# Kernel optimization log

Measured on AMD Instinct MI355X. Metric: run time of the kernel, lower is better.

The kernel has to match this reference:

```python
import jax, jax.numpy as jnp
import numpy as np

B, C, H, W_ = 64, 512, 32, 32


def setup_inputs() -> dict:
    key = jax.random.key(0)
    k0, k1, k2, k3 = jax.random.split(key, 4)
    x = jax.random.normal(k0, (B, C, H, W_), dtype=jnp.float32)
    # conv1x1 weight [3c, c] (kernel dims of size 1 squeezed)
    W = jax.random.normal(k1, (3 * C, C), dtype=jnp.float32) * 0.02
    rel_h = jax.random.normal(k2, (1, C, H, 1), dtype=jnp.float32)
    rel_w = jax.random.normal(k3, (1, C, 1, W_), dtype=jnp.float32)
    return {"x": x, "W": W, "rel_h": rel_h, "rel_w": rel_w}


def reference(x, W, rel_h, rel_w):
    b, c, h, w = x.shape
    n = h * w
    xf = x.reshape(b, c, n)
    # 1x1 conv == channel matmul: [b, 3c, n]
    qkv = jnp.einsum('oc,bcn->bon', W, xf)
    q, k, v = jnp.split(qkv, 3, axis=1)  # each [b, c, n]
    # content-content: q^T k -> [b, n, n]
    content_content = jnp.einsum('bcn,bcm->bnm', q, k)
    # relative position bias: pos [c, n]; pos^T @ q -> [b, n, n]
    pos = (rel_h + rel_w).reshape(c, n)
    content_position = jnp.einsum('cn,bcm->bnm', pos, q)
    attention = jax.nn.softmax(content_content + content_position, axis=-1)
    # out = bmm(v, attention^T) -> [b, c, n]
    out = jnp.einsum('bcm,bnm->bcn', v, attention)
    return out.reshape(b, c, h, w)
```

## Files before the change

kernel.cpp:

```cpp
#include <hip/hip_runtime.h>

#define B_    64
#define C_    512
#define H_    32
#define WDIM  32
#define N_    1024
#define M3C   1536

typedef unsigned short ushort_t;
typedef __attribute__((ext_vector_type(8))) short bf16x8;
typedef __attribute__((ext_vector_type(4))) float f32x4;

__device__ __forceinline__ ushort_t f2bf(float x) {
    unsigned u = __float_as_uint(x);
    unsigned r = (u + 0x7FFFu + ((u >> 16) & 1u)) >> 16;
    return (ushort_t)r;
}
__device__ __forceinline__ float bf2f(ushort_t b) {
    return __uint_as_float(((unsigned)b) << 16);
}
__device__ __forceinline__ void split_write(float v, ushort_t* __restrict__ ph,
                                            ushort_t* __restrict__ pl, size_t idx) {
    ushort_t hb = f2bf(v);
    ph[idx] = hb;
    pl[idx] = f2bf(v - bf2f(hb));
}

__device__ __forceinline__ void gld16(const void* g, void* l) {
    __builtin_amdgcn_global_load_lds((const __attribute__((address_space(1))) unsigned int*)g,
                                     (__attribute__((address_space(3))) unsigned int*)l,
                                     16, 0, 0);
}

__global__ __launch_bounds__(256) void pos_kernel(const float* __restrict__ rel_h,
                                                  const float* __restrict__ rel_w,
                                                  float* __restrict__ pos) {
    int idx = blockIdx.x * 256 + threadIdx.x;
    if (idx >= C_ * N_) return;
    int c = idx >> 10;
    int n = idx & (N_ - 1);
    int h = n >> 5;
    int w = n & (WDIM - 1);
    pos[idx] = rel_h[c * H_ + h] + rel_w[c * WDIM + w];
}

__global__ __launch_bounds__(256) void mmT_f32(const float* __restrict__ A, int lda,
                                               const float* __restrict__ B, int ldb,
                                               float* __restrict__ D, int ldd, int K) {
    __shared__ float As[16][64];
    __shared__ float Bs[16][64];
    const int m0 = blockIdx.y * 64;
    const int n0 = blockIdx.x * 64;
    const int tx = threadIdx.x, ty = threadIdx.y;
    const int tid = ty * 16 + tx;
    float acc[4][4] = {};
    for (int k0 = 0; k0 < K; k0 += 16) {
        #pragma unroll
        for (int t = 0; t < 4; ++t) {
            int e = tid + t * 256;
            int j = e >> 6, i = e & 63;
            As[j][i] = A[(size_t)(k0 + j) * lda + m0 + i];
            Bs[j][i] = B[(size_t)(k0 + j) * ldb + n0 + i];
        }
        __syncthreads();
        #pragma unroll
        for (int kk = 0; kk < 16; ++kk) {
            float a[4], bb[4];
            #pragma unroll
            for (int i = 0; i < 4; ++i) a[i]  = As[kk][ty * 4 + i];
            #pragma unroll
            for (int j = 0; j < 4; ++j) bb[j] = Bs[kk][tx * 4 + j];
            #pragma unroll
            for (int i = 0; i < 4; ++i)
                #pragma unroll
                for (int j = 0; j < 4; ++j)
                    acc[i][j] += a[i] * bb[j];
        }
        __syncthreads();
    }
    #pragma unroll
    for (int i = 0; i < 4; ++i)
        #pragma unroll
        for (int j = 0; j < 4; ++j)
            D[(size_t)(m0 + ty * 4 + i) * ldd + n0 + tx * 4 + j] = acc[i][j];
}

__global__ __launch_bounds__(256) void f_split(const float* __restrict__ Mtmp,
                                               const float* __restrict__ Wm,
                                               ushort_t* __restrict__ Fh,
                                               ushort_t* __restrict__ Fl) {
    int idx = blockIdx.x * 256 + threadIdx.x;
    if (idx >= 1024 * C_) return;
    int o = idx >> 9;
    int c = idx & (C_ - 1);
    float v = (o < 512) ? Mtmp[idx] : Wm[(size_t)(512 + o) * C_ + c];
    split_write(v, Fh, Fl, idx);
}

__global__ __launch_bounds__(256) void xT_split(const float* __restrict__ x,
                                                ushort_t* __restrict__ xh,
                                                ushort_t* __restrict__ xl) {
    __shared__ float t[32][33];
    const int bl = blockIdx.z;
    const int c0 = blockIdx.y * 32;
    const int n0 = blockIdx.x * 32;
    const float* xb = x + (size_t)bl * C_ * N_;
    ushort_t* xhb = xh + (size_t)bl * N_ * C_;
    ushort_t* xlb = xl + (size_t)bl * N_ * C_;
    const int tx = threadIdx.x & 31, ty = threadIdx.x >> 5;
    #pragma unroll
    for (int r = 0; r < 4; ++r)
        t[ty + r * 8][tx] = xb[(size_t)(c0 + ty + r * 8) * N_ + n0 + tx];
    __syncthreads();
    #pragma unroll
    for (int r = 0; r < 4; ++r) {
        float v = t[tx][ty + r * 8];
        size_t o = (size_t)(n0 + ty + r * 8) * C_ + c0 + tx;
        split_write(v, xhb, xlb, o);
    }
}


__global__ __launch_bounds__(512, 2) void g1_mfma(const ushort_t* __restrict__ Fh_,
                                                  const ushort_t* __restrict__ Fl_,
                                                  const ushort_t* __restrict__ xTh_,
                                                  const ushort_t* __restrict__ xTl_,
                                                  ushort_t* __restrict__ tTh_,
                                                  ushort_t* __restrict__ tTl_,
                                                  ushort_t* __restrict__ vh_,
                                                  ushort_t* __restrict__ vl_) {
    __shared__ ushort_t lds[2][4][2][4096];
    const int bl = blockIdx.z;
    const int n0 = blockIdx.x * 256;
    const int m0 = blockIdx.y * 256;
    const char* Ah = (const char*)Fh_;
    const char* Al = (const char*)Fl_;
    const char* Bh = (const char*)(xTh_ + (size_t)bl * N_ * C_);
    const char* Bl = (const char*)(xTl_ + (size_t)bl * N_ * C_);

    const int tid = threadIdx.x;
    const int lane = tid & 63, wid = tid >> 6;
    const int wr = wid >> 2, wc = wid & 3;
    const int lr = lane & 15, g = lane >> 4;
    const int cswz = g ^ ((lr >> 1) & 3);
    const int offA = lr * 32 + cswz * 8;
    const int offB = ((wc & 1) * 64 + lr) * 32 + cswz * 8;
    const int srow = tid >> 2;
    const int toff = srow * 1024 + (((tid & 3) ^ ((srow >> 1) & 3)) << 4);
    const int ldst = wid * 512;

    f32x4 acc[8][4] = {};

#define G1_ISSUE_A(buf, kb) \
    gld16(Ah + (size_t)(m0)       * 1024 + (kb) + toff, &lds[buf][0][0][ldst]); \
    gld16(Ah + (size_t)(m0 + 128) * 1024 + (kb) + toff, &lds[buf][0][1][ldst]); \
    gld16(Al + (size_t)(m0)       * 1024 + (kb) + toff, &lds[buf][1][0][ldst]); \
    gld16(Al + (size_t)(m0 + 128) * 1024 + (kb) + toff, &lds[buf][1][1][ldst]);
#define G1_ISSUE_B(buf, kb) \
    gld16(Bh + (size_t)(n0)       * 1024 + (kb) + toff, &lds[buf][2][0][ldst]); \
    gld16(Bh + (size_t)(n0 + 128) * 1024 + (kb) + toff, &lds[buf][2][1][ldst]); \
    gld16(Bl + (size_t)(n0)       * 1024 + (kb) + toff, &lds[buf][3][0][ldst]); \
    gld16(Bl + (size_t)(n0 + 128) * 1024 + (kb) + toff, &lds[buf][3][1][ldst]);

    G1_ISSUE_A(0, 0);
    G1_ISSUE_B(0, 0);
    asm volatile("s_waitcnt vmcnt(0)" ::: "memory");
    __builtin_amdgcn_s_barrier();

    bf16x8 bfh[4], bfl[4];
    for (int t = 0; t < 16; ++t) {
        const int cur = t & 1, nxt = cur ^ 1;
        const bool pf = (t < 15);
        const int nk = (t + 1) * 64;
        #pragma unroll
        for (int p = 0; p < 4; ++p) {
            if (p == 0) {
                #pragma unroll
                for (int j = 0; j < 4; ++j) {
                    bfh[j] = *(const bf16x8*)&lds[cur][2][wc >> 1][j * 512 + offB];
                    bfl[j] = *(const bf16x8*)&lds[cur][3][wc >> 1][j * 512 + offB];
                }
            }
            bf16x8 ah0 = *(const bf16x8*)&lds[cur][0][wr][(p * 2 + 0) * 512 + offA];
            bf16x8 al0 = *(const bf16x8*)&lds[cur][1][wr][(p * 2 + 0) * 512 + offA];
            bf16x8 ah1 = *(const bf16x8*)&lds[cur][0][wr][(p * 2 + 1) * 512 + offA];
            bf16x8 al1 = *(const bf16x8*)&lds[cur][1][wr][(p * 2 + 1) * 512 + offA];
            if (pf && p == 0) { G1_ISSUE_A(nxt, nk); }
            if (pf && p == 1) { G1_ISSUE_B(nxt, nk); }
            __builtin_amdgcn_s_barrier();
            asm volatile("s_waitcnt lgkmcnt(0)" ::: "memory");
            __builtin_amdgcn_s_setprio(1);
            #pragma unroll
            for (int j = 0; j < 4; ++j) {
                acc[p*2+0][j] = __builtin_amdgcn_mfma_f32_16x16x32_bf16(ah0, bfh[j], acc[p*2+0][j], 0,0,0);
                acc[p*2+0][j] = __builtin_amdgcn_mfma_f32_16x16x32_bf16(ah0, bfl[j], acc[p*2+0][j], 0,0,0);
                acc[p*2+0][j] = __builtin_amdgcn_mfma_f32_16x16x32_bf16(al0, bfh[j], acc[p*2+0][j], 0,0,0);
                acc[p*2+1][j] = __builtin_amdgcn_mfma_f32_16x16x32_bf16(ah1, bfh[j], acc[p*2+1][j], 0,0,0);
                acc[p*2+1][j] = __builtin_amdgcn_mfma_f32_16x16x32_bf16(ah1, bfl[j], acc[p*2+1][j], 0,0,0);
                acc[p*2+1][j] = __builtin_amdgcn_mfma_f32_16x16x32_bf16(al1, bfh[j], acc[p*2+1][j], 0,0,0);
            }
            __builtin_amdgcn_s_setprio(0);
            if (p == 3) asm volatile("s_waitcnt vmcnt(0)" ::: "memory");
            __builtin_amdgcn_s_barrier();
        }
    }
#undef G1_ISSUE_A
#undef G1_ISSUE_B

    if (m0 < 512) {
        ushort_t* th = tTh_ + (size_t)bl * N_ * C_;
        ushort_t* tl = tTl_ + (size_t)bl * N_ * C_;
        #pragma unroll
        for (int i = 0; i < 8; ++i) {
            int ob = m0 + wr * 128 + i * 16 + g * 4;
            #pragma unroll
            for (int j = 0; j < 4; ++j) {
                int n = n0 + wc * 64 + j * 16 + lr;
                ushort4 h4, l4;
                ushort_t hb;
                float v0 = acc[i][j][0], v1 = acc[i][j][1], v2 = acc[i][j][2], v3 = acc[i][j][3];
                hb = f2bf(v0); h4.x = hb; l4.x = f2bf(v0 - bf2f(hb));
                hb = f2bf(v1); h4.y = hb; l4.y = f2bf(v1 - bf2f(hb));
                hb = f2bf(v2); h4.z = hb; l4.z = f2bf(v2 - bf2f(hb));
                hb = f2bf(v3); h4.w = hb; l4.w = f2bf(v3 - bf2f(hb));
                *reinterpret_cast<ushort4*>(&th[(size_t)n * C_ + ob]) = h4;
                *reinterpret_cast<ushort4*>(&tl[(size_t)n * C_ + ob]) = l4;
            }
        }
    } else {
        ushort_t* vh = vh_ + (size_t)bl * C_ * N_;
        ushort_t* vl = vl_ + (size_t)bl * C_ * N_;
        #pragma unroll
        for (int i = 0; i < 8; ++i) {
            int cb = m0 - 512 + wr * 128 + i * 16 + g * 4;
            #pragma unroll
            for (int j = 0; j < 4; ++j) {
                int m = n0 + wc * 64 + j * 16 + lr;
                #pragma unroll
                for (int r = 0; r < 4; ++r) {
                    float v = acc[i][j][r];
                    ushort_t hb = f2bf(v);
                    vh[(size_t)(cb + r) * N_ + m] = hb;
                    vl[(size_t)(cb + r) * N_ + m] = f2bf(v - bf2f(hb));
                }
            }
        }
    }
}

__global__ __launch_bounds__(512, 2) void g2_mfma(const ushort_t* __restrict__ xTh_,
                                                  const ushort_t* __restrict__ xTl_,
                                                  const ushort_t* __restrict__ rTh_,
                                                  const ushort_t* __restrict__ rTl_,
                                                  const ushort_t* __restrict__ tTh_,
                                                  const ushort_t* __restrict__ tTl_,
                                                  float* __restrict__ S) {
    __shared__ ushort_t lds[2][4][2][4096];
    const int bl = blockIdx.z;
    const int m0 = blockIdx.x * 256;
    const int n0 = blockIdx.y * 256;
    const char* xh = (const char*)(xTh_ + (size_t)bl * N_ * C_);
    const char* xl = (const char*)(xTl_ + (size_t)bl * N_ * C_);
    const char* th = (const char*)(tTh_ + (size_t)bl * N_ * C_);
    const char* tl = (const char*)(tTl_ + (size_t)bl * N_ * C_);
    const char* rh = (const char*)rTh_;
    const char* rl = (const char*)rTl_;

    const int tid = threadIdx.x;
    const int lane = tid & 63, wid = tid >> 6;
    const int wr = wid >> 2, wc = wid & 3;
    const int lr = lane & 15, g = lane >> 4;
    const int cswz = g ^ ((lr >> 1) & 3);
    const int offA = lr * 32 + cswz * 8;
    const int offB = ((wc & 1) * 64 + lr) * 32 + cswz * 8;
    const int srow = tid >> 2;
    const int toff = srow * 1024 + (((tid & 3) ^ ((srow >> 1) & 3)) << 4);
    const int ldst = wid * 512;

    f32x4 acc[8][4] = {};

#define G2_SRC(s, vAh, vAl, vBh, vBl, vk) \
    const char *vAh, *vAl, *vBh, *vBl; int vk; \
    if ((s) < 16) { vAh = xh; vAl = xl; vBh = th; vBl = tl; vk = (s) * 64; } \
    else          { vAh = rh; vAl = rl; vBh = xh; vBl = xl; vk = ((s) - 16) * 64; }
#define G2_ISSUE_A(buf, vAh, vAl, vk) \
    gld16(vAh + (size_t)(n0)       * 1024 + (vk) + toff, &lds[buf][0][0][ldst]); \
    gld16(vAh + (size_t)(n0 + 128) * 1024 + (vk) + toff, &lds[buf][0][1][ldst]); \
    gld16(vAl + (size_t)(n0)       * 1024 + (vk) + toff, &lds[buf][1][0][ldst]); \
    gld16(vAl + (size_t)(n0 + 128) * 1024 + (vk) + toff, &lds[buf][1][1][ldst]);
#define G2_ISSUE_B(buf, vBh, vBl, vk) \
    gld16(vBh + (size_t)(m0)       * 1024 + (vk) + toff, &lds[buf][2][0][ldst]); \
    gld16(vBh + (size_t)(m0 + 128) * 1024 + (vk) + toff, &lds[buf][2][1][ldst]); \
    gld16(vBl + (size_t)(m0)       * 1024 + (vk) + toff, &lds[buf][3][0][ldst]); \
    gld16(vBl + (size_t)(m0 + 128) * 1024 + (vk) + toff, &lds[buf][3][1][ldst]);

    {
        G2_SRC(0, pAh, pAl, pBh, pBl, pk);
        G2_ISSUE_A(0, pAh, pAl, pk);
        G2_ISSUE_B(0, pBh, pBl, pk);
        asm volatile("s_waitcnt vmcnt(0)" ::: "memory");
        __builtin_amdgcn_s_barrier();
    }

    bf16x8 bfh[4], bfl[4];
    for (int t = 0; t < 32; ++t) {
        const int cur = t & 1, nxt = cur ^ 1;
        const bool pf = (t < 31);
        G2_SRC(t + 1, nAh, nAl, nBh, nBl, nk);
        #pragma unroll
        for (int p = 0; p < 4; ++p) {
            if (p == 0) {
                #pragma unroll
                for (int j = 0; j < 4; ++j) {
                    bfh[j] = *(const bf16x8*)&lds[cur][2][wc >> 1][j * 512 + offB];
                    bfl[j] = *(const bf16x8*)&lds[cur][3][wc >> 1][j * 512 + offB];
                }
            }
            bf16x8 ah0 = *(const bf16x8*)&lds[cur][0][wr][(p * 2 + 0) * 512 + offA];
            bf16x8 al0 = *(const bf16x8*)&lds[cur][1][wr][(p * 2 + 0) * 512 + offA];
            bf16x8 ah1 = *(const bf16x8*)&lds[cur][0][wr][(p * 2 + 1) * 512 + offA];
            bf16x8 al1 = *(const bf16x8*)&lds[cur][1][wr][(p * 2 + 1) * 512 + offA];
            if (pf && p == 0) { G2_ISSUE_A(nxt, nAh, nAl, nk); }
            if (pf && p == 1) { G2_ISSUE_B(nxt, nBh, nBl, nk); }
            __builtin_amdgcn_s_barrier();
            asm volatile("s_waitcnt lgkmcnt(0)" ::: "memory");
            __builtin_amdgcn_s_setprio(1);
            #pragma unroll
            for (int j = 0; j < 4; ++j) {
                acc[p*2+0][j] = __builtin_amdgcn_mfma_f32_16x16x32_bf16(ah0, bfh[j], acc[p*2+0][j], 0,0,0);
                acc[p*2+0][j] = __builtin_amdgcn_mfma_f32_16x16x32_bf16(ah0, bfl[j], acc[p*2+0][j], 0,0,0);
                acc[p*2+0][j] = __builtin_amdgcn_mfma_f32_16x16x32_bf16(al0, bfh[j], acc[p*2+0][j], 0,0,0);
                acc[p*2+1][j] = __builtin_amdgcn_mfma_f32_16x16x32_bf16(ah1, bfh[j], acc[p*2+1][j], 0,0,0);
                acc[p*2+1][j] = __builtin_amdgcn_mfma_f32_16x16x32_bf16(ah1, bfl[j], acc[p*2+1][j], 0,0,0);
                acc[p*2+1][j] = __builtin_amdgcn_mfma_f32_16x16x32_bf16(al1, bfh[j], acc[p*2+1][j], 0,0,0);
            }
            __builtin_amdgcn_s_setprio(0);
            if (p == 3) asm volatile("s_waitcnt vmcnt(0)" ::: "memory");
            __builtin_amdgcn_s_barrier();
        }
    }
#undef G2_SRC
#undef G2_ISSUE_A
#undef G2_ISSUE_B

    float* Sb = S + (size_t)bl * N_ * N_;
    #pragma unroll
    for (int i = 0; i < 8; ++i) {
        int n = n0 + wr * 128 + i * 16 + g * 4;
        #pragma unroll
        for (int j = 0; j < 4; ++j) {
            int m = m0 + wc * 64 + j * 16 + lr;
            #pragma unroll
            for (int r = 0; r < 4; ++r)
                Sb[(size_t)(n + r) * N_ + m] = acc[i][j][r];
        }
    }
}

__device__ __forceinline__ float waveMax(float v) {
    #pragma unroll
    for (int o = 32; o > 0; o >>= 1) v = fmaxf(v, __shfl_down(v, o));
    return v;
}
__device__ __forceinline__ float waveSum(float v) {
    #pragma unroll
    for (int o = 32; o > 0; o >>= 1) v += __shfl_down(v, o);
    return v;
}

__global__ __launch_bounds__(256) void softmax_bf16(const float* __restrict__ S,
                                                    ushort_t* __restrict__ P) {
    const float* Sr = S + (size_t)blockIdx.x * N_;
    ushort_t* Pr = P + (size_t)blockIdx.x * N_;
    const int tid = threadIdx.x;
    float4 v = reinterpret_cast<const float4*>(Sr)[tid];
    __shared__ float redm[4];
    __shared__ float reds[4];
    const int wave = tid >> 6, lane = tid & 63;

    float m = fmaxf(fmaxf(v.x, v.y), fmaxf(v.z, v.w));
    m = waveMax(m);
    if (lane == 0) redm[wave] = m;
    __syncthreads();
    m = fmaxf(fmaxf(redm[0], redm[1]), fmaxf(redm[2], redm[3]));

    v.x = __expf(v.x - m); v.y = __expf(v.y - m);
    v.z = __expf(v.z - m); v.w = __expf(v.w - m);
    float s = v.x + v.y + v.z + v.w;
    s = waveSum(s);
    if (lane == 0) reds[wave] = s;
    __syncthreads();
    s = reds[0] + reds[1] + reds[2] + reds[3];
    const float inv = 1.0f / s;
    ushort4 p;
    p.x = f2bf(v.x * inv); p.y = f2bf(v.y * inv);
    p.z = f2bf(v.z * inv); p.w = f2bf(v.w * inv);
    reinterpret_cast<ushort4*>(Pr)[tid] = p;
}

__global__ __launch_bounds__(512, 2) void g4_mfma(const ushort_t* __restrict__ vh_,
                                                  const ushort_t* __restrict__ vl_,
                                                  const ushort_t* __restrict__ P_,
                                                  float* __restrict__ out) {
    __shared__ ushort_t lds[2][3][2][4096];
    const int bl = blockIdx.z;
    const int n0 = blockIdx.x * 256;
    const int c0 = blockIdx.y * 256;
    const char* Ah = (const char*)(vh_ + (size_t)bl * C_ * N_);
    const char* Al = (const char*)(vl_ + (size_t)bl * C_ * N_);
    const char* Bp = (const char*)(P_ + (size_t)bl * N_ * N_);

    const int tid = threadIdx.x;
    const int lane = tid & 63, wid = tid >> 6;
    const int wr = wid >> 2, wc = wid & 3;
    const int lr = lane & 15, g = lane >> 4;
    const int cswz = g ^ ((lr >> 1) & 3);
    const int offA = lr * 32 + cswz * 8;
    const int offB = ((wc & 1) * 64 + lr) * 32 + cswz * 8;
    const int srow = tid >> 2;
    const int toff = srow * 2048 + (((tid & 3) ^ ((srow >> 1) & 3)) << 4);
    const int ldst = wid * 512;

    f32x4 acc[8][4] = {};

#define G4_ISSUE_A(buf, kb) \
    gld16(Ah + (size_t)(c0)       * 2048 + (kb) + toff, &lds[buf][0][0][ldst]); \
    gld16(Ah + (size_t)(c0 + 128) * 2048 + (kb) + toff, &lds[buf][0][1][ldst]); \
    gld16(Al + (size_t)(c0)       * 2048 + (kb) + toff, &lds[buf][1][0][ldst]); \
    gld16(Al + (size_t)(c0 + 128) * 2048 + (kb) + toff, &lds[buf][1][1][ldst]);
#define G4_ISSUE_B(buf, kb) \
    gld16(Bp + (size_t)(n0)       * 2048 + (kb) + toff, &lds[buf][2][0][ldst]); \
    gld16(Bp + (size_t)(n0 + 128) * 2048 + (kb) + toff, &lds[buf][2][1][ldst]);

    G4_ISSUE_A(0, 0);
    G4_ISSUE_B(0, 0);
    asm volatile("s_waitcnt vmcnt(0)" ::: "memory");
    __builtin_amdgcn_s_barrier();

    bf16x8 bf[4];
    for (int t = 0; t < 32; ++t) {
        const int cur = t & 1, nxt = cur ^ 1;
        const bool pf = (t < 31);
        const int nk = (t + 1) * 64;
        #pragma unroll
        for (int p = 0; p < 4; ++p) {
            if (p == 0) {
                #pragma unroll
                for (int j = 0; j < 4; ++j)
                    bf[j] = *(const bf16x8*)&lds[cur][2][wc >> 1][j * 512 + offB];
            }
            bf16x8 ah0 = *(const bf16x8*)&lds[cur][0][wr][(p * 2 + 0) * 512 + offA];
            bf16x8 al0 = *(const bf16x8*)&lds[cur][1][wr][(p * 2 + 0) * 512 + offA];
            bf16x8 ah1 = *(const bf16x8*)&lds[cur][0][wr][(p * 2 + 1) * 512 + offA];
            bf16x8 al1 = *(const bf16x8*)&lds[cur][1][wr][(p * 2 + 1) * 512 + offA];
            if (pf && p == 0) { G4_ISSUE_A(nxt, nk); }
            if (pf && p == 1) { G4_ISSUE_B(nxt, nk); }
            __builtin_amdgcn_s_barrier();
            asm volatile("s_waitcnt lgkmcnt(0)" ::: "memory");
            __builtin_amdgcn_s_setprio(1);
            #pragma unroll
            for (int j = 0; j < 4; ++j) {
                acc[p*2+0][j] = __builtin_amdgcn_mfma_f32_16x16x32_bf16(ah0, bf[j], acc[p*2+0][j], 0,0,0);
                acc[p*2+0][j] = __builtin_amdgcn_mfma_f32_16x16x32_bf16(al0, bf[j], acc[p*2+0][j], 0,0,0);
                acc[p*2+1][j] = __builtin_amdgcn_mfma_f32_16x16x32_bf16(ah1, bf[j], acc[p*2+1][j], 0,0,0);
                acc[p*2+1][j] = __builtin_amdgcn_mfma_f32_16x16x32_bf16(al1, bf[j], acc[p*2+1][j], 0,0,0);
            }
            __builtin_amdgcn_s_setprio(0);
            if (p == 3) asm volatile("s_waitcnt vmcnt(0)" ::: "memory");
            __builtin_amdgcn_s_barrier();
        }
    }
#undef G4_ISSUE_A
#undef G4_ISSUE_B

    float* ob = out + (size_t)bl * C_ * N_;
    #pragma unroll
    for (int i = 0; i < 8; ++i) {
        int c = c0 + wr * 128 + i * 16 + g * 4;
        #pragma unroll
        for (int j = 0; j < 4; ++j) {
            int n = n0 + wc * 64 + j * 16 + lr;
            #pragma unroll
            for (int r = 0; r < 4; ++r)
                ob[(size_t)(c + r) * N_ + n] = acc[i][j][r];
        }
    }
}

extern "C" void kernel_launch(void* const* d_in, const int* in_sizes, int n_in,
                              void* d_out, int out_size, void* d_ws, size_t ws_size,
                              hipStream_t stream) {
    const float* x     = (const float*)d_in[0];
    const float* Wm    = (const float*)d_in[1];
    const float* rel_h = (const float*)d_in[2];
    const float* rel_w = (const float*)d_in[3];
    float* out = (float*)d_out;

    const size_t posB  = (size_t)C_ * N_ * 4;
    const size_t MtB   = (size_t)C_ * C_ * 4;
    const size_t rtB   = (size_t)C_ * N_ * 4;
    const size_t fplB  = (size_t)1024 * C_ * 2;
    const size_t rtplB = (size_t)N_ * C_ * 2;
    const size_t xtB   = (size_t)N_ * C_ * 2;
    const size_t ttB   = (size_t)N_ * C_ * 2;
    const size_t vplB  = (size_t)C_ * N_ * 2;
    const size_t sB    = (size_t)N_ * N_ * 4;
    const size_t pB    = (size_t)N_ * N_ * 2;
    const size_t per_batch = 2 * xtB + 2 * ttB + 2 * vplB + sB + pB;
    const size_t persist   = posB + MtB + rtB + 2 * fplB + 2 * rtplB;

    size_t rem = (ws_size > persist) ? (ws_size - persist) : 0;
    int chunkB = (int)(rem / per_batch);
    if (chunkB < 1)  chunkB = 1;
    if (chunkB > B_) chunkB = B_;

    char* p = (char*)d_ws;
    float*    pos  = (float*)p;    p += posB;
    float*    Mtmp = (float*)p;    p += MtB;
    float*    rtmp = (float*)p;    p += rtB;
    ushort_t* Fh   = (ushort_t*)p; p += fplB;
    ushort_t* Fl   = (ushort_t*)p; p += fplB;
    ushort_t* rTh  = (ushort_t*)p; p += rtplB;
    ushort_t* rTl  = (ushort_t*)p; p += rtplB;
    ushort_t* xTh  = (ushort_t*)p; p += (size_t)chunkB * xtB;
    ushort_t* xTl  = (ushort_t*)p; p += (size_t)chunkB * xtB;
    ushort_t* tTh  = (ushort_t*)p; p += (size_t)chunkB * ttB;
    ushort_t* tTl  = (ushort_t*)p; p += (size_t)chunkB * ttB;
    ushort_t* vh   = (ushort_t*)p; p += (size_t)chunkB * vplB;
    ushort_t* vl   = (ushort_t*)p; p += (size_t)chunkB * vplB;
    float*    S    = (float*)p;    p += (size_t)chunkB * sB;
    ushort_t* P    = (ushort_t*)p; p += (size_t)chunkB * pB;

    dim3 blk16(16, 16);
    pos_kernel<<<(C_ * N_ + 255) / 256, 256, 0, stream>>>(rel_h, rel_w, pos);
    mmT_f32<<<dim3(C_ / 64, C_ / 64), blk16, 0, stream>>>(Wm, C_, Wm + (size_t)C_ * C_, C_,
                                                          Mtmp, C_, C_);
    mmT_f32<<<dim3(N_ / 64, C_ / 64), blk16, 0, stream>>>(Wm, C_, pos, N_, rtmp, N_, C_);
    f_split<<<(1024 * C_ + 255) / 256, 256, 0, stream>>>(Mtmp, Wm, Fh, Fl);
    xT_split<<<dim3(N_ / 32, C_ / 32, 1), 256, 0, stream>>>(rtmp, rTh, rTl);

    for (int b0 = 0; b0 < B_; b0 += chunkB) {
        int nb = (b0 + chunkB <= B_) ? chunkB : (B_ - b0);
        const float* x_b   = x   + (size_t)b0 * C_ * N_;
        float*       out_b = out + (size_t)b0 * C_ * N_;
        xT_split<<<dim3(N_ / 32, C_ / 32, nb), 256, 0, stream>>>(x_b, xTh, xTl);
        g1_mfma<<<dim3(4, 4, nb), 512, 0, stream>>>(Fh, Fl, xTh, xTl, tTh, tTl, vh, vl);
        g2_mfma<<<dim3(4, 4, nb), 512, 0, stream>>>(xTh, xTl, rTh, rTl, tTh, tTl, S);
        softmax_bf16<<<nb * N_, 256, 0, stream>>>(S, P);
        g4_mfma<<<dim3(4, 2, nb), 512, 0, stream>>>(vh, vl, P, out_b);
    }
}
```

Baseline: 1.261 ms.

## Switch GEMM kernels to 32x32x16 MFMA with two-stage-ahead prefetch pipeline

```diff
diff --git a/kernel.cpp b/kernel.cpp
--- a/kernel.cpp
+++ b/kernel.cpp
@@ -10,6 +10,9 @@
 typedef unsigned short ushort_t;
 typedef __attribute__((ext_vector_type(8))) short bf16x8;
 typedef __attribute__((ext_vector_type(4))) float f32x4;
+typedef __attribute__((ext_vector_type(16))) float f32x16;
+
+#define MEMFENCE asm volatile("" ::: "memory")
 
 __device__ __forceinline__ ushort_t f2bf(float x) {
     unsigned u = __float_as_uint(x);
@@ -141,110 +144,114 @@
     const int tid = threadIdx.x;
     const int lane = tid & 63, wid = tid >> 6;
     const int wr = wid >> 2, wc = wid & 3;
-    const int lr = lane & 15, g = lane >> 4;
-    const int cswz = g ^ ((lr >> 1) & 3);
-    const int offA = lr * 32 + cswz * 8;
-    const int offB = ((wc & 1) * 64 + lr) * 32 + cswz * 8;
+    const int l31 = lane & 31, l5 = lane >> 5;
+    const int swz4 = (l31 >> 1) & 3;
+    const int chk0 = ((l5)     ^ swz4) << 3;
+    const int chk1 = ((2 | l5) ^ swz4) << 3;
     const int srow = tid >> 2;
     const int toff = srow * 1024 + (((tid & 3) ^ ((srow >> 1) & 3)) << 4);
     const int ldst = wid * 512;
 
-    f32x4 acc[8][4] = {};
-
-#define G1_ISSUE_A(buf, kb) \
+    f32x16 acc[4][2] = {};
+
+#define G1_ISSUE(buf, kb) \
     gld16(Ah + (size_t)(m0)       * 1024 + (kb) + toff, &lds[buf][0][0][ldst]); \
     gld16(Ah + (size_t)(m0 + 128) * 1024 + (kb) + toff, &lds[buf][0][1][ldst]); \
     gld16(Al + (size_t)(m0)       * 1024 + (kb) + toff, &lds[buf][1][0][ldst]); \
-    gld16(Al + (size_t)(m0 + 128) * 1024 + (kb) + toff, &lds[buf][1][1][ldst]);
-#define G1_ISSUE_B(buf, kb) \
+    gld16(Al + (size_t)(m0 + 128) * 1024 + (kb) + toff, &lds[buf][1][1][ldst]); \
     gld16(Bh + (size_t)(n0)       * 1024 + (kb) + toff, &lds[buf][2][0][ldst]); \
     gld16(Bh + (size_t)(n0 + 128) * 1024 + (kb) + toff, &lds[buf][2][1][ldst]); \
     gld16(Bl + (size_t)(n0)       * 1024 + (kb) + toff, &lds[buf][3][0][ldst]); \
     gld16(Bl + (size_t)(n0 + 128) * 1024 + (kb) + toff, &lds[buf][3][1][ldst]);
 
-    G1_ISSUE_A(0, 0);
-    G1_ISSUE_B(0, 0);
-    asm volatile("s_waitcnt vmcnt(0)" ::: "memory");
-    __builtin_amdgcn_s_barrier();
-
-    bf16x8 bfh[4], bfl[4];
+    G1_ISSUE(0, 0);
+    G1_ISSUE(1, 64);
+    int cur = 0;
     for (int t = 0; t < 16; ++t) {
-        const int cur = t & 1, nxt = cur ^ 1;
-        const bool pf = (t < 15);
-        const int nk = (t + 1) * 64;
-        #pragma unroll
-        for (int p = 0; p < 4; ++p) {
-            if (p == 0) {
-                #pragma unroll
-                for (int j = 0; j < 4; ++j) {
-                    bfh[j] = *(const bf16x8*)&lds[cur][2][wc >> 1][j * 512 + offB];
-                    bfl[j] = *(const bf16x8*)&lds[cur][3][wc >> 1][j * 512 + offB];
-                }
-            }
-            bf16x8 ah0 = *(const bf16x8*)&lds[cur][0][wr][(p * 2 + 0) * 512 + offA];
-            bf16x8 al0 = *(const bf16x8*)&lds[cur][1][wr][(p * 2 + 0) * 512 + offA];
-            bf16x8 ah1 = *(const bf16x8*)&lds[cur][0][wr][(p * 2 + 1) * 512 + offA];
-            bf16x8 al1 = *(const bf16x8*)&lds[cur][1][wr][(p * 2 + 1) * 512 + offA];
-            if (pf && p == 0) { G1_ISSUE_A(nxt, nk); }
-            if (pf && p == 1) { G1_ISSUE_B(nxt, nk); }
-            __builtin_amdgcn_s_barrier();
-            asm volatile("s_waitcnt lgkmcnt(0)" ::: "memory");
+        if (t + 1 < 16) asm volatile("s_waitcnt vmcnt(8)" ::: "memory");
+        else            asm volatile("s_waitcnt vmcnt(0)" ::: "memory");
+        __builtin_amdgcn_s_barrier();
+        MEMFENCE;
+        bf16x8 bh[2][2], bo[2][2];
+        #pragma unroll
+        for (int j = 0; j < 2; ++j) {
+            int br = ((wc & 1) * 64 + j * 32 + l31) * 32;
+            bh[j][0] = *(const bf16x8*)&lds[cur][2][wc >> 1][br + chk0];
+            bh[j][1] = *(const bf16x8*)&lds[cur][2][wc >> 1][br + chk1];
+            bo[j][0] = *(const bf16x8*)&lds[cur][3][wc >> 1][br + chk0];
+            bo[j][1] = *(const bf16x8*)&lds[cur][3][wc >> 1][br + chk1];
+        }
+        #pragma unroll
+        for (int i = 0; i < 4; ++i) {
+            int ar = (i * 32 + l31) * 32;
+            bf16x8 ah0 = *(const bf16x8*)&lds[cur][0][wr][ar + chk0];
+            bf16x8 ah1 = *(const bf16x8*)&lds[cur][0][wr][ar + chk1];
+            bf16x8 al0 = *(const bf16x8*)&lds[cur][1][wr][ar + chk0];
+            bf16x8 al1 = *(const bf16x8*)&lds[cur][1][wr][ar + chk1];
             __builtin_amdgcn_s_setprio(1);
             #pragma unroll
-            for (int j = 0; j < 4; ++j) {
-                acc[p*2+0][j] = __builtin_amdgcn_mfma_f32_16x16x32_bf16(ah0, bfh[j], acc[p*2+0][j], 0,0,0);
-                acc[p*2+0][j] = __builtin_amdgcn_mfma_f32_16x16x32_bf16(ah0, bfl[j], acc[p*2+0][j], 0,0,0);
-                acc[p*2+0][j] = __builtin_amdgcn_mfma_f32_16x16x32_bf16(al0, bfh[j], acc[p*2+0][j], 0,0,0);
-                acc[p*2+1][j] = __builtin_amdgcn_mfma_f32_16x16x32_bf16(ah1, bfh[j], acc[p*2+1][j], 0,0,0);
-                acc[p*2+1][j] = __builtin_amdgcn_mfma_f32_16x16x32_bf16(ah1, bfl[j], acc[p*2+1][j], 0,0,0);
-                acc[p*2+1][j] = __builtin_amdgcn_mfma_f32_16x16x32_bf16(al1, bfh[j], acc[p*2+1][j], 0,0,0);
+            for (int j = 0; j < 2; ++j) {
+                acc[i][j] = __builtin_amdgcn_mfma_f32_32x32x16_bf16(ah0, bh[j][0], acc[i][j], 0,0,0);
+                acc[i][j] = __builtin_amdgcn_mfma_f32_32x32x16_bf16(ah0, bo[j][0], acc[i][j], 0,0,0);
+                acc[i][j] = __builtin_amdgcn_mfma_f32_32x32x16_bf16(al0, bh[j][0], acc[i][j], 0,0,0);
+                acc[i][j] = __builtin_amdgcn_mfma_f32_32x32x16_bf16(ah1, bh[j][1], acc[i][j], 0,0,0);
+                acc[i][j] = __builtin_amdgcn_mfma_f32_32x32x16_bf16(ah1, bo[j][1], acc[i][j], 0,0,0);
+                acc[i][j] = __builtin_amdgcn_mfma_f32_32x32x16_bf16(al1, bh[j][1], acc[i][j], 0,0,0);
             }
             __builtin_amdgcn_s_setprio(0);
-            if (p == 3) asm volatile("s_waitcnt vmcnt(0)" ::: "memory");
-            __builtin_amdgcn_s_barrier();
-        }
-    }
-#undef G1_ISSUE_A
-#undef G1_ISSUE_B
+        }
+        asm volatile("s_waitcnt lgkmcnt(0)" ::: "memory");
+        __builtin_amdgcn_sched_barrier(0);
+        __builtin_amdgcn_s_barrier();
+        MEMFENCE;
+        if (t + 2 < 16) { G1_ISSUE(cur, (t + 2) * 64); }
+        cur ^= 1;
+    }
+#undef G1_ISSUE
 
     if (m0 < 512) {
         ushort_t* th = tTh_ + (size_t)bl * N_ * C_;
         ushort_t* tl = tTl_ + (size_t)bl * N_ * C_;
         #pragma unroll
-        for (int i = 0; i < 8; ++i) {
-            int ob = m0 + wr * 128 + i * 16 + g * 4;
-            #pragma unroll
-            for (int j = 0; j < 4; ++j) {
-                int n = n0 + wc * 64 + j * 16 + lr;
-                ushort4 h4, l4;
-                ushort_t hb;
-                float v0 = acc[i][j][0], v1 = acc[i][j][1], v2 = acc[i][j][2], v3 = acc[i][j][3];
-                hb = f2bf(v0); h4.x = hb; l4.x = f2bf(v0 - bf2f(hb));
-                hb = f2bf(v1); h4.y = hb; l4.y = f2bf(v1 - bf2f(hb));
-                hb = f2bf(v2); h4.z = hb; l4.z = f2bf(v2 - bf2f(hb));
-                hb = f2bf(v3); h4.w = hb; l4.w = f2bf(v3 - bf2f(hb));
-                *reinterpret_cast<ushort4*>(&th[(size_t)n * C_ + ob]) = h4;
-                *reinterpret_cast<ushort4*>(&tl[(size_t)n * C_ + ob]) = l4;
-            }
-        }
+        for (int i = 0; i < 4; ++i)
+            #pragma unroll
+            for (int j = 0; j < 2; ++j) {
+                int n = n0 + wc * 64 + j * 32 + l31;
+                #pragma unroll
+                for (int q = 0; q < 4; ++q) {
+                    int o = m0 + wr * 128 + i * 32 + q * 8 + l5 * 4;
+                    ushort4 h4, l4;
+                    ushort_t hb;
+                    float v0 = acc[i][j][q*4+0], v1 = acc[i][j][q*4+1];
+                    float v2 = acc[i][j][q*4+2], v3 = acc[i][j][q*4+3];
+                    hb = f2bf(v0); h4.x = hb; l4.x = f2bf(v0 - bf2f(hb));
+                    hb = f2bf(v1); h4.y = hb; l4.y = f2bf(v1 - bf2f(hb));
+                    hb = f2bf(v2); h4.z = hb; l4.z = f2bf(v2 - bf2f(hb));
+                    hb = f2bf(v3); h4.w = hb; l4.w = f2bf(v3 - bf2f(hb));
+                    *reinterpret_cast<ushort4*>(&th[(size_t)n * C_ + o]) = h4;
+                    *reinterpret_cast<ushort4*>(&tl[(size_t)n * C_ + o]) = l4;
+                }
+            }
     } else {
         ushort_t* vh = vh_ + (size_t)bl * C_ * N_;
         ushort_t* vl = vl_ + (size_t)bl * C_ * N_;
         #pragma unroll
-        for (int i = 0; i < 8; ++i) {
-            int cb = m0 - 512 + wr * 128 + i * 16 + g * 4;
-            #pragma unroll
-            for (int j = 0; j < 4; ++j) {
-                int m = n0 + wc * 64 + j * 16 + lr;
+        for (int i = 0; i < 4; ++i)
+            #pragma unroll
+            for (int j = 0; j < 2; ++j) {
+                int m = n0 + wc * 64 + j * 32 + l31;
                 #pragma unroll
-                for (int r = 0; r < 4; ++r) {
-                    float v = acc[i][j][r];
-                    ushort_t hb = f2bf(v);
-                    vh[(size_t)(cb + r) * N_ + m] = hb;
-                    vl[(size_t)(cb + r) * N_ + m] = f2bf(v - bf2f(hb));
+                for (int q = 0; q < 4; ++q) {
+                    int cb = m0 - 512 + wr * 128 + i * 32 + q * 8 + l5 * 4;
+                    #pragma unroll
+                    for (int rr = 0; rr < 4; ++rr) {
+                        float v = acc[i][j][q*4+rr];
+                        ushort_t hb = f2bf(v);
+                        vh[(size_t)(cb + rr) * N_ + m] = hb;
+                        vl[(size_t)(cb + rr) * N_ + m] = f2bf(v - bf2f(hb));
+                    }
                 }
             }
-        }
     }
 }
 
@@ -269,92 +276,93 @@
     const int tid = threadIdx.x;
     const int lane = tid & 63, wid = tid >> 6;
     const int wr = wid >> 2, wc = wid & 3;
-    const int lr = lane & 15, g = lane >> 4;
-    const int cswz = g ^ ((lr >> 1) & 3);
-    const int offA = lr * 32 + cswz * 8;
-    const int offB = ((wc & 1) * 64 + lr) * 32 + cswz * 8;
+    const int l31 = lane & 31, l5 = lane >> 5;
+    const int swz4 = (l31 >> 1) & 3;
+    const int chk0 = ((l5)     ^ swz4) << 3;
+    const int chk1 = ((2 | l5) ^ swz4) << 3;
     const int srow = tid >> 2;
     const int toff = srow * 1024 + (((tid & 3) ^ ((srow >> 1) & 3)) << 4);
     const int ldst = wid * 512;
 
-    f32x4 acc[8][4] = {};
-
-#define G2_SRC(s, vAh, vAl, vBh, vBl, vk) \
-    const char *vAh, *vAl, *vBh, *vBl; int vk; \
-    if ((s) < 16) { vAh = xh; vAl = xl; vBh = th; vBl = tl; vk = (s) * 64; } \
-    else          { vAh = rh; vAl = rl; vBh = xh; vBl = xl; vk = ((s) - 16) * 64; }
-#define G2_ISSUE_A(buf, vAh, vAl, vk) \
-    gld16(vAh + (size_t)(n0)       * 1024 + (vk) + toff, &lds[buf][0][0][ldst]); \
-    gld16(vAh + (size_t)(n0 + 128) * 1024 + (vk) + toff, &lds[buf][0][1][ldst]); \
-    gld16(vAl + (size_t)(n0)       * 1024 + (vk) + toff, &lds[buf][1][0][ldst]); \
-    gld16(vAl + (size_t)(n0 + 128) * 1024 + (vk) + toff, &lds[buf][1][1][ldst]);
-#define G2_ISSUE_B(buf, vBh, vBl, vk) \
-    gld16(vBh + (size_t)(m0)       * 1024 + (vk) + toff, &lds[buf][2][0][ldst]); \
-    gld16(vBh + (size_t)(m0 + 128) * 1024 + (vk) + toff, &lds[buf][2][1][ldst]); \
-    gld16(vBl + (size_t)(m0)       * 1024 + (vk) + toff, &lds[buf][3][0][ldst]); \
-    gld16(vBl + (size_t)(m0 + 128) * 1024 + (vk) + toff, &lds[buf][3][1][ldst]);
-
-    {
-        G2_SRC(0, pAh, pAl, pBh, pBl, pk);
-        G2_ISSUE_A(0, pAh, pAl, pk);
-        G2_ISSUE_B(0, pBh, pBl, pk);
-        asm volatile("s_waitcnt vmcnt(0)" ::: "memory");
+    f32x16 acc[4][2] = {};
+
+#define G2_ISSUE(buf, pAh, pAl, pBh, pBl, kb) \
+    gld16(pAh + (size_t)(n0)       * 1024 + (kb) + toff, &lds[buf][0][0][ldst]); \
+    gld16(pAh + (size_t)(n0 + 128) * 1024 + (kb) + toff, &lds[buf][0][1][ldst]); \
+    gld16(pAl + (size_t)(n0)       * 1024 + (kb) + toff, &lds[buf][1][0][ldst]); \
+    gld16(pAl + (size_t)(n0 + 128) * 1024 + (kb) + toff, &lds[buf][1][1][ldst]); \
+    gld16(pBh + (size_t)(m0)       * 1024 + (kb) + toff, &lds[buf][2][0][ldst]); \
+    gld16(pBh + (size_t)(m0 + 128) * 1024 + (kb) + toff, &lds[buf][2][1][ldst]); \
+    gld16(pBl + (size_t)(m0)       * 1024 + (kb) + toff, &lds[buf][3][0][ldst]); \
+    gld16(pBl + (size_t)(m0 + 128) * 1024 + (kb) + toff, &lds[buf][3][1][ldst]);
+
+    G2_ISSUE(0, xh, xl, th, tl, 0);
+    G2_ISSUE(1, xh, xl, th, tl, 64);
+    int cur = 0;
+    for (int t = 0; t < 32; ++t) {
+        if (t + 1 < 32) asm volatile("s_waitcnt vmcnt(8)" ::: "memory");
+        else            asm volatile("s_waitcnt vmcnt(0)" ::: "memory");
         __builtin_amdgcn_s_barrier();
-    }
-
-    bf16x8 bfh[4], bfl[4];
-    for (int t = 0; t < 32; ++t) {
-        const int cur = t & 1, nxt = cur ^ 1;
-        const bool pf = (t < 31);
-        G2_SRC(t + 1, nAh, nAl, nBh, nBl, nk);
-        #pragma unroll
-        for (int p = 0; p < 4; ++p) {
-            if (p == 0) {
+        MEMFENCE;
+        bf16x8 bh[2][2], bo[2][2];
+        #pragma unroll
+        for (int j = 0; j < 2; ++j) {
+            int br = ((wc & 1) * 64 + j * 32 + l31) * 32;
+            bh[j][0] = *(const bf16x8*)&lds[cur][2][wc >> 1][br + chk0];
+            bh[j][1] = *(const bf16x8*)&lds[cur][2][wc >> 1][br + chk1];
+            bo[j][0] = *(const bf16x8*)&lds[cur][3][wc >> 1][br + chk0];
+            bo[j][1] = *(const bf16x8*)&lds[cur][3][wc >> 1][br + chk1];
+        }
+        #pragma unroll
+        for (int i = 0; i < 4; ++i) {
+            int ar = (i * 32 + l31) * 32;
+            bf16x8 ah0 = *(const bf16x8*)&lds[cur][0][wr][ar + chk0];
+            bf16x8 ah1 = *(const bf16x8*)&lds[cur][0][wr][ar + chk1];
+            bf16x8 al0 = *(const bf16x8*)&lds[cur][1][wr][ar + chk0];
+            bf16x8 al1 = *(const bf16x8*)&lds[cur][1][wr][ar + chk1];
+            __builtin_amdgcn_s_setprio(1);
+            #pragma unroll
+            for (int j = 0; j < 2; ++j) {
+                acc[i][j] = __builtin_amdgcn_mfma_f32_32x32x16_bf16(ah0, bh[j][0], acc[i][j], 0,0,0);
+                acc[i][j] = __builtin_amdgcn_mfma_f32_32x32x16_bf16(ah0, bo[j][0], acc[i][j], 0,0,0);
+                acc[i][j] = __builtin_amdgcn_mfma_f32_32x32x16_bf16(al0, bh[j][0], acc[i][j], 0,0,0);
+                acc[i][j] = __builtin_amdgcn_mfma_f32_32x32x16_bf16(ah1, bh[j][1], acc[i][j], 0,0,0);
+                acc[i][j] = __builtin_amdgcn_mfma_f32_32x32x16_bf16(ah1, bo[j][1], acc[i][j], 0,0,0);
+                acc[i][j] = __builtin_amdgcn_mfma_f32_32x32x16_bf16(al1, bh[j][1], acc[i][j], 0,0,0);
+            }
+            __builtin_amdgcn_s_setprio(0);
+        }
+        asm volatile("s_waitcnt lgkmcnt(0)" ::: "memory");
+        __builtin_amdgcn_sched_barrier(0);
+        __builtin_amdgcn_s_barrier();
+        MEMFENCE;
+        if (t + 2 < 32) {
+            int s = t + 2;
+            const char* pAh = (s < 16) ? xh : rh;
+            const char* pAl = (s < 16) ? xl : rl;
+            const char* pBh = (s < 16) ? th : xh;
+            const char* pBl = (s < 16) ? tl : xl;
+            int kb = (s & 15) * 64;
+            G2_ISSUE(cur, pAh, pAl, pBh, pBl, kb);
+        }
+        cur ^= 1;
+    }
+#undef G2_ISSUE
+
+    float* Sb = S + (size_t)bl * N_ * N_;
+    #pragma unroll
+    for (int i = 0; i < 4; ++i)
+        #pragma unroll
+        for (int j = 0; j < 2; ++j) {
+            int m = m0 + wc * 64 + j * 32 + l31;
+            #pragma unroll
+            for (int q = 0; q < 4; ++q) {
+                int n = n0 + wr * 128 + i * 32 + q * 8 + l5 * 4;
                 #pragma unroll
-                for (int j = 0; j < 4; ++j) {
-                    bfh[j] = *(const bf16x8*)&lds[cur][2][wc >> 1][j * 512 + offB];
-                    bfl[j] = *(const bf16x8*)&lds[cur][3][wc >> 1][j * 512 + offB];
-                }
-            }
-            bf16x8 ah0 = *(const bf16x8*)&lds[cur][0][wr][(p * 2 + 0) * 512 + offA];
-            bf16x8 al0 = *(const bf16x8*)&lds[cur][1][wr][(p * 2 + 0) * 512 + offA];
-            bf16x8 ah1 = *(const bf16x8*)&lds[cur][0][wr][(p * 2 + 1) * 512 + offA];
-            bf16x8 al1 = *(const bf16x8*)&lds[cur][1][wr][(p * 2 + 1) * 512 + offA];
-            if (pf && p == 0) { G2_ISSUE_A(nxt, nAh, nAl, nk); }
-            if (pf && p == 1) { G2_ISSUE_B(nxt, nBh, nBl, nk); }
-            __builtin_amdgcn_s_barrier();
-            asm volatile("s_waitcnt lgkmcnt(0)" ::: "memory");
-            __builtin_amdgcn_s_setprio(1);
-            #pragma unroll
-            for (int j = 0; j < 4; ++j) {
-                acc[p*2+0][j] = __builtin_amdgcn_mfma_f32_16x16x32_bf16(ah0, bfh[j], acc[p*2+0][j], 0,0,0);
-                acc[p*2+0][j] = __builtin_amdgcn_mfma_f32_16x16x32_bf16(ah0, bfl[j], acc[p*2+0][j], 0,0,0);
-                acc[p*2+0][j] = __builtin_amdgcn_mfma_f32_16x16x32_bf16(al0, bfh[j], acc[p*2+0][j], 0,0,0);
-                acc[p*2+1][j] = __builtin_amdgcn_mfma_f32_16x16x32_bf16(ah1, bfh[j], acc[p*2+1][j], 0,0,0);
-                acc[p*2+1][j] = __builtin_amdgcn_mfma_f32_16x16x32_bf16(ah1, bfl[j], acc[p*2+1][j], 0,0,0);
-                acc[p*2+1][j] = __builtin_amdgcn_mfma_f32_16x16x32_bf16(al1, bfh[j], acc[p*2+1][j], 0,0,0);
-            }
-            __builtin_amdgcn_s_setprio(0);
-            if (p == 3) asm volatile("s_waitcnt vmcnt(0)" ::: "memory");
-            __builtin_amdgcn_s_barrier();
-        }
-    }
-#undef G2_SRC
-#undef G2_ISSUE_A
-#undef G2_ISSUE_B
-
-    float* Sb = S + (size_t)bl * N_ * N_;
-    #pragma unroll
-    for (int i = 0; i < 8; ++i) {
-        int n = n0 + wr * 128 + i * 16 + g * 4;
-        #pragma unroll
-        for (int j = 0; j < 4; ++j) {
-            int m = m0 + wc * 64 + j * 16 + lr;
-            #pragma unroll
-            for (int r = 0; r < 4; ++r)
-                Sb[(size_t)(n + r) * N_ + m] = acc[i][j][r];
-        }
-    }
+                for (int rr = 0; rr < 4; ++rr)
+                    Sb[(size_t)(n + rr) * N_ + m] = acc[i][j][q*4+rr];
+            }
+        }
 }
 
 __device__ __forceinline__ float waveMax(float v) {
@@ -413,78 +421,79 @@
     const int tid = threadIdx.x;
     const int lane = tid & 63, wid = tid >> 6;
     const int wr = wid >> 2, wc = wid & 3;
-    const int lr = lane & 15, g = lane >> 4;
-    const int cswz = g ^ ((lr >> 1) & 3);
-    const int offA = lr * 32 + cswz * 8;
-    const int offB = ((wc & 1) * 64 + lr) * 32 + cswz * 8;
+    const int l31 = lane & 31, l5 = lane >> 5;
+    const int swz4 = (l31 >> 1) & 3;
+    const int chk0 = ((l5)     ^ swz4) << 3;
+    const int chk1 = ((2 | l5) ^ swz4) << 3;
     const int srow = tid >> 2;
     const int toff = srow * 2048 + (((tid & 3) ^ ((srow >> 1) & 3)) << 4);
     const int ldst = wid * 512;
 
-    f32x4 acc[8][4] = {};
-
-#define G4_ISSUE_A(buf, kb) \
+    f32x16 acc[4][2] = {};
+
+#define G4_ISSUE(buf, kb) \
     gld16(Ah + (size_t)(c0)       * 2048 + (kb) + toff, &lds[buf][0][0][ldst]); \
     gld16(Ah + (size_t)(c0 + 128) * 2048 + (kb) + toff, &lds[buf][0][1][ldst]); \
     gld16(Al + (size_t)(c0)       * 2048 + (kb) + toff, &lds[buf][1][0][ldst]); \
-    gld16(Al + (size_t)(c0 + 128) * 2048 + (kb) + toff, &lds[buf][1][1][ldst]);
-#define G4_ISSUE_B(buf, kb) \
+    gld16(Al + (size_t)(c0 + 128) * 2048 + (kb) + toff, &lds[buf][1][1][ldst]); \
     gld16(Bp + (size_t)(n0)       * 2048 + (kb) + toff, &lds[buf][2][0][ldst]); \
     gld16(Bp + (size_t)(n0 + 128) * 2048 + (kb) + toff, &lds[buf][2][1][ldst]);
 
-    G4_ISSUE_A(0, 0);
-    G4_ISSUE_B(0, 0);
-    asm volatile("s_waitcnt vmcnt(0)" ::: "memory");
-    __builtin_amdgcn_s_barrier();
-
-    bf16x8 bf[4];
+    G4_ISSUE(0, 0);
+    G4_ISSUE(1, 64);
+    int cur = 0;
     for (int t = 0; t < 32; ++t) {
-        const int cur = t & 1, nxt = cur ^ 1;
-        const bool pf = (t < 31);
-        const int nk = (t + 1) * 64;
-        #pragma unroll
-        for (int p = 0; p < 4; ++p) {
-            if (p == 0) {
+        if (t + 1 < 32) asm volatile("s_waitcnt vmcnt(6)" ::: "memory");
+        else            asm volatile("s_waitcnt vmcnt(0)" ::: "memory");
+        __builtin_amdgcn_s_barrier();
+        MEMFENCE;
+        bf16x8 bf[2][2];
+        #pragma unroll
+        for (int j = 0; j < 2; ++j) {
+            int br = ((wc & 1) * 64 + j * 32 + l31) * 32;
+            bf[j][0] = *(const bf16x8*)&lds[cur][2][wc >> 1][br + chk0];
+            bf[j][1] = *(const bf16x8*)&lds[cur][2][wc >> 1][br + chk1];
+        }
+        #pragma unroll
+        for (int i = 0; i < 4; ++i) {
+            int ar = (i * 32 + l31) * 32;
+            bf16x8 ah0 = *(const bf16x8*)&lds[cur][0][wr][ar + chk0];
+            bf16x8 ah1 = *(const bf16x8*)&lds[cur][0][wr][ar + chk1];
+            bf16x8 al0 = *(const bf16x8*)&lds[cur][1][wr][ar + chk0];
+            bf16x8 al1 = *(const bf16x8*)&lds[cur][1][wr][ar + chk1];
+            __builtin_amdgcn_s_setprio(1);
+            #pragma unroll
+            for (int j = 0; j < 2; ++j) {
+                acc[i][j] = __builtin_amdgcn_mfma_f32_32x32x16_bf16(ah0, bf[j][0], acc[i][j], 0,0,0);
+                acc[i][j] = __builtin_amdgcn_mfma_f32_32x32x16_bf16(al0, bf[j][0], acc[i][j], 0,0,0);
+                acc[i][j] = __builtin_amdgcn_mfma_f32_32x32x16_bf16(ah1, bf[j][1], acc[i][j], 0,0,0);
+                acc[i][j] = __builtin_amdgcn_mfma_f32_32x32x16_bf16(al1, bf[j][1], acc[i][j], 0,0,0);
+            }
+            __builtin_amdgcn_s_setprio(0);
+        }
+        asm volatile("s_waitcnt lgkmcnt(0)" ::: "memory");
+        __builtin_amdgcn_sched_barrier(0);
+        __builtin_amdgcn_s_barrier();
+        MEMFENCE;
+        if (t + 2 < 32) { G4_ISSUE(cur, (t + 2) * 64); }
+        cur ^= 1;
+    }
+#undef G4_ISSUE
+
+    float* ob = out + (size_t)bl * C_ * N_;
+    #pragma unroll
+    for (int i = 0; i < 4; ++i)
+        #pragma unroll
+        for (int j = 0; j < 2; ++j) {
+            int n = n0 + wc * 64 + j * 32 + l31;
+            #pragma unroll
+            for (int q = 0; q < 4; ++q) {
+                int c = c0 + wr * 128 + i * 32 + q * 8 + l5 * 4;
                 #pragma unroll
-                for (int j = 0; j < 4; ++j)
-                    bf[j] = *(const bf16x8*)&lds[cur][2][wc >> 1][j * 512 + offB];
-            }
-            bf16x8 ah0 = *(const bf16x8*)&lds[cur][0][wr][(p * 2 + 0) * 512 + offA];
-            bf16x8 al0 = *(const bf16x8*)&lds[cur][1][wr][(p * 2 + 0) * 512 + offA];
-            bf16x8 ah1 = *(const bf16x8*)&lds[cur][0][wr][(p * 2 + 1) * 512 + offA];
-            bf16x8 al1 = *(const bf16x8*)&lds[cur][1][wr][(p * 2 + 1) * 512 + offA];
-            if (pf && p == 0) { G4_ISSUE_A(nxt, nk); }
-            if (pf && p == 1) { G4_ISSUE_B(nxt, nk); }
-            __builtin_amdgcn_s_barrier();
-            asm volatile("s_waitcnt lgkmcnt(0)" ::: "memory");
-            __builtin_amdgcn_s_setprio(1);
-            #pragma unroll
-            for (int j = 0; j < 4; ++j) {
-                acc[p*2+0][j] = __builtin_amdgcn_mfma_f32_16x16x32_bf16(ah0, bf[j], acc[p*2+0][j], 0,0,0);
-                acc[p*2+0][j] = __builtin_amdgcn_mfma_f32_16x16x32_bf16(al0, bf[j], acc[p*2+0][j], 0,0,0);
-                acc[p*2+1][j] = __builtin_amdgcn_mfma_f32_16x16x32_bf16(ah1, bf[j], acc[p*2+1][j], 0,0,0);
-                acc[p*2+1][j] = __builtin_amdgcn_mfma_f32_16x16x32_bf16(al1, bf[j], acc[p*2+1][j], 0,0,0);
-            }
-            __builtin_amdgcn_s_setprio(0);
-            if (p == 3) asm volatile("s_waitcnt vmcnt(0)" ::: "memory");
-            __builtin_amdgcn_s_barrier();
-        }
-    }
-#undef G4_ISSUE_A
-#undef G4_ISSUE_B
-
-    float* ob = out + (size_t)bl * C_ * N_;
-    #pragma unroll
-    for (int i = 0; i < 8; ++i) {
-        int c = c0 + wr * 128 + i * 16 + g * 4;
-        #pragma unroll
-        for (int j = 0; j < 4; ++j) {
-            int n = n0 + wc * 64 + j * 16 + lr;
-            #pragma unroll
-            for (int r = 0; r < 4; ++r)
-                ob[(size_t)(c + r) * N_ + n] = acc[i][j][r];
-        }
-    }
+                for (int rr = 0; rr < 4; ++rr)
+                    ob[(size_t)(c + rr) * N_ + n] = acc[i][j][q*4+rr];
+            }
+        }
 }
 
 extern "C" void kernel_launch(void* const* d_in, const int* in_sizes, int n_in,
```

After: 1.332 ms. 1.06x slower.
